# Performance work log

Measured on AMD Instinct MI355X. Metric: run time of the kernel, lower is better.

## Reference

```python
import jax, jax.numpy as jnp
import numpy as np

N, E, C, D_E, G = 50000, 800000, 64, 32, 512


def setup_inputs() -> dict:
    key = jax.random.key(0)
    ks = jax.random.split(key, 12)
    inp = {
        "x": jax.random.normal(ks[0], (N, C), dtype=jnp.float32),
        "edge_index": jax.random.randint(ks[1], (2, E), 0, N, dtype=jnp.int64),
        "edge_attr": jax.random.normal(ks[2], (E, D_E), dtype=jnp.float32),
        "batch": jnp.sort(jax.random.randint(ks[3], (N,), 0, G, dtype=jnp.int64)),
        "num_graphs": G,
        # CGConv gating linears: Linear(2*C + D_E, C)
        "W_f": jax.random.normal(ks[4], (2 * C + D_E, C), dtype=jnp.float32) * 0.05,
        "b_f": jnp.zeros((C,), dtype=jnp.float32),
        "W_s": jax.random.normal(ks[5], (2 * C + D_E, C), dtype=jnp.float32) * 0.05,
        "b_s": jnp.zeros((C,), dtype=jnp.float32),
        # head MLP
        "W1": jax.random.normal(ks[6], (C, 6), dtype=jnp.float32) * 0.1,
        "b1": jnp.zeros((6,), dtype=jnp.float32),
        "W2": jax.random.normal(ks[7], (6, 1), dtype=jnp.float32) * 0.1,
        "b2": jnp.zeros((1,), dtype=jnp.float32),
    }
    return inp


def cg_conv(x, edge_index, edge_attr, W_f, b_f, W_s, b_s):
    src, dst = edge_index[0], edge_index[1]
    # PyG CGConv message: z = cat([x_i (dst), x_j (src), edge_attr])
    z = jnp.concatenate([x[dst], x[src], edge_attr], axis=-1)  # [E, 2C+D]
    msg = jax.nn.sigmoid(z @ W_f + b_f) * jax.nn.softplus(z @ W_s + b_s)  # [E, C]
    agg = jax.ops.segment_sum(msg, dst, num_segments=x.shape[0])  # scatter-add to dst
    return x + agg  # residual


def reference(x, edge_index, edge_attr, batch, num_graphs, W_f, b_f, W_s, b_s, W1, b1, W2, b2):
    h = cg_conv(x, edge_index, edge_attr, W_f, b_f, W_s, b_s)  # [N, C]
    h = jax.nn.sigmoid(h)
    h = jax.nn.sigmoid(h @ W1 + b1)  # [N, 6]
    g = jax.ops.segment_sum(h, batch, num_segments=num_graphs)  # global_add_pool [G, 6]
    out = jax.nn.relu(g @ W2 + b2)  # [G, 1]
    return out
```

## Files before the change

### kernel.cpp

```cpp
#include <hip/hip_runtime.h>
#include <hip/hip_bf16.h>
#include <stdint.h>

#define NN 50000
#define EE 800000
#define CC 64
#define DE 32
#define KD 160
#define NC 128
#define GG 512
#define SCAN_B 1024
#define NSCAN ((NN + SCAN_B - 1) / SCAN_B)

typedef __attribute__((ext_vector_type(8))) short bf16x8;
typedef __attribute__((ext_vector_type(4))) float f32x4;

__device__ __forceinline__ float sigmoidf_(float v) {
  return __fdividef(1.f, 1.f + __expf(-v));
}
__device__ __forceinline__ float softplusf_(float v) {
  return fmaxf(v, 0.f) + __logf(1.f + __expf(-fabsf(v)));
}
__device__ __forceinline__ unsigned short f2bf(float f) {
  uint32_t u = __float_as_uint(f);
  return (unsigned short)((u + 0x7FFFu + ((u >> 16) & 1u)) >> 16);
}
__device__ __forceinline__ float bf2f(unsigned short h) {
  return __uint_as_float(((uint32_t)h) << 16);
}
__device__ __forceinline__ void tsplit(float f, short& hi, short& lo) {
  uint32_t u = __float_as_uint(f);
  float lf = f - __uint_as_float(u & 0xFFFF0000u);
  hi = (short)(u >> 16);
  lo = (short)(__float_as_uint(lf) >> 16);
}

__global__ void count_kernel(const int* __restrict__ ei, int* __restrict__ deg) {
  int e = blockIdx.x * 256 + threadIdx.x;
  atomicAdd(&deg[ei[EE + e]], 1);
}

__global__ __launch_bounds__(SCAN_B) void scan1_kernel(
    const int* __restrict__ deg, int* __restrict__ pos, int* __restrict__ bsum) {
  __shared__ int s[SCAN_B];
  int t = threadIdx.x, i = blockIdx.x * SCAN_B + t;
  s[t] = (i < NN) ? deg[i] : 0;
  __syncthreads();
  for (int off = 1; off < SCAN_B; off <<= 1) {
    int a = (t >= off) ? s[t - off] : 0;
    __syncthreads();
    s[t] += a;
    __syncthreads();
  }
  if (i < NN) pos[i + 1] = s[t];
  if (t == SCAN_B - 1) bsum[blockIdx.x] = s[t];
}

__global__ void scan2_kernel(int* __restrict__ bsum) {
  __shared__ int s[64];
  int t = threadIdx.x;
  s[t] = (t < NSCAN) ? bsum[t] : 0;
  __syncthreads();
  for (int off = 1; off < 64; off <<= 1) {
    int a = (t >= off) ? s[t - off] : 0;
    __syncthreads();
    s[t] += a;
    __syncthreads();
  }
  bsum[t] = (t == 0) ? 0 : s[t - 1];
}

__global__ __launch_bounds__(SCAN_B) void scan3_kernel(
    int* __restrict__ pos, const int* __restrict__ bsum, int* __restrict__ cursor) {
  int t = threadIdx.x, i = blockIdx.x * SCAN_B + t;
  if (i < NN) {
    int v = pos[i + 1] + bsum[blockIdx.x];
    pos[i + 1] = v;
    if (i + 1 < NN) cursor[i + 1] = v;
  }
  if (i == 0) { pos[0] = 0; cursor[0] = 0; }
}

__global__ void fill_kernel(const int* __restrict__ ei, int* __restrict__ cursor,
                            int* __restrict__ eidx, int* __restrict__ dsts,
                            int* __restrict__ srcs) {
  int e = blockIdx.x * 256 + threadIdx.x;
  int d = ei[EE + e];
  int s = ei[e];
  int slot = atomicAdd(&cursor[d], 1);
  eidx[slot] = e;
  dsts[slot] = d;
  srcs[slot] = s;
}

__global__ void xsplit_kernel(const float* __restrict__ x,
                              unsigned short* __restrict__ xhi,
                              unsigned short* __restrict__ xlo) {
  int idx = blockIdx.x * 256 + threadIdx.x;
  float4 v = ((const float4*)x)[idx];
  ushort4 h, l;
  short a, b;
  tsplit(v.x, a, b); h.x = (unsigned short)a; l.x = (unsigned short)b;
  tsplit(v.y, a, b); h.y = (unsigned short)a; l.y = (unsigned short)b;
  tsplit(v.z, a, b); h.z = (unsigned short)a; l.z = (unsigned short)b;
  tsplit(v.w, a, b); h.w = (unsigned short)a; l.w = (unsigned short)b;
  *(ushort4*)(xhi + (size_t)idx * 4) = h;
  *(ushort4*)(xlo + (size_t)idx * 4) = l;
}

__global__ void wprep_kernel(const float* __restrict__ Wf, const float* __restrict__ Ws,
                             short* __restrict__ Bph, short* __restrict__ Bpl) {
  int p = blockIdx.x * 256 + threadIdx.x;
  int i = p & 7, l = (p >> 3) & 63, tile = p >> 9;
  int nt = tile & 7, s = tile >> 3;
  int k = s * 32 + 8 * (l >> 4) + i;
  int col = nt * 16 + (l & 15);
  float w = (col < CC) ? Wf[k * CC + col] : Ws[k * CC + (col - CC)];
  short hi, lo;
  tsplit(w, hi, lo);
  Bph[p] = hi;
  Bpl[p] = lo;
}

template <bool BF16MSG>
__global__ __launch_bounds__(512) void edge_mfma_kernel(
    const unsigned short* __restrict__ xhi, const unsigned short* __restrict__ xlo,
    const int* __restrict__ eidx, const int* __restrict__ dsts,
    const int* __restrict__ srcs, const float* __restrict__ ea,
    const short* __restrict__ Bph, const short* __restrict__ Bpl,
    const float* __restrict__ bfv, const float* __restrict__ bsv,
    void* __restrict__ msg)
{
  __shared__ short Bh[20480];
  const int t = threadIdx.x;

  {
    const float4* gh = (const float4*)Bph;
    float4* sh = (float4*)Bh;
    #pragma unroll
    for (int r = 0; r < 5; ++r) sh[r * 512 + t] = gh[r * 512 + t];
  }

  const int w  = t >> 6, l = t & 63;
  const int mg = w >> 1, ng = w & 1;
  const int sbase = blockIdx.x * 256 + mg * 64;
  const int lr = l & 15, lg = l >> 4;

  int dst[4], src[4], ep[4];
  #pragma unroll
  for (int mt = 0; mt < 4; ++mt) {
    const int slot = sbase + mt * 16 + lr;
    dst[mt] = dsts[slot];
    src[mt] = srcs[slot];
    ep[mt]  = eidx[slot];
  }
  __syncthreads();

  f32x4 acc[4][4];
  #pragma unroll
  for (int mt = 0; mt < 4; ++mt)
    #pragma unroll
    for (int q = 0; q < 4; ++q) acc[mt][q] = (f32x4){0.f, 0.f, 0.f, 0.f};

  const bf16x8* Blg = (const bf16x8*)Bpl;

  #pragma unroll
  for (int s = 0; s < 5; ++s) {
    bf16x8 ah[4], al[4];
    if (s < 4) {
      const int koff = (s & 1) * 32 + 8 * lg;
      #pragma unroll
      for (int mt = 0; mt < 4; ++mt) {
        const int row = (s < 2) ? dst[mt] : src[mt];
        const size_t o = (size_t)row * CC + koff;
        ah[mt] = *(const bf16x8*)(xhi + o);
        al[mt] = *(const bf16x8*)(xlo + o);
      }
    } else {
      #pragma unroll
      for (int mt = 0; mt < 4; ++mt) {
        const float4* p4 = (const float4*)(ea + (size_t)ep[mt] * DE + 8 * lg);
        float4 v0 = p4[0], v1 = p4[1];
        float v[8] = {v0.x, v0.y, v0.z, v0.w, v1.x, v1.y, v1.z, v1.w};
        #pragma unroll
        for (int i = 0; i < 8; ++i) {
          short hh, ll;
          tsplit(v[i], hh, ll);
          ah[mt][i] = hh;
          al[mt][i] = ll;
        }
      }
    }
    bf16x8 bh[4], bl[4];
    #pragma unroll
    for (int q = 0; q < 4; ++q) {
      const int nt  = 2 * ng + (q & 1) + (q >> 1) * 4;
      bh[q] = *(const bf16x8*)(Bh + ((s * 8 + nt) * 64 + l) * 8);
      bl[q] = Blg[(s * 8 + nt) * 64 + l];
    }
    #pragma unroll
    for (int mt = 0; mt < 4; ++mt)
      #pragma unroll
      for (int q = 0; q < 4; ++q)
        acc[mt][q] = __builtin_amdgcn_mfma_f32_16x16x32_bf16(ah[mt], bh[q], acc[mt][q], 0, 0, 0);
    #pragma unroll
    for (int mt = 0; mt < 4; ++mt)
      #pragma unroll
      for (int q = 0; q < 4; ++q)
        acc[mt][q] = __builtin_amdgcn_mfma_f32_16x16x32_bf16(al[mt], bh[q], acc[mt][q], 0, 0, 0);
    #pragma unroll
    for (int mt = 0; mt < 4; ++mt)
      #pragma unroll
      for (int q = 0; q < 4; ++q)
        acc[mt][q] = __builtin_amdgcn_mfma_f32_16x16x32_bf16(ah[mt], bl[q], acc[mt][q], 0, 0, 0);
  }

  #pragma unroll
  for (int p2 = 0; p2 < 2; ++p2) {
    const int ch = (2 * ng + p2) * 16 + lr;
    const float bF = bfv[ch], bS = bsv[ch];
    #pragma unroll
    for (int mt = 0; mt < 4; ++mt) {
      f32x4 F = acc[mt][p2];
      f32x4 S = acc[mt][p2 + 2];
      #pragma unroll
      for (int r = 0; r < 4; ++r) {
        const int oslot = sbase + mt * 16 + lg * 4 + r;
        const float mval = sigmoidf_(F[r] + bF) * softplusf_(S[r] + bS);
        if constexpr (!BF16MSG) {
          ((float*)msg)[(size_t)oslot * CC + ch] = mval;
        } else {
          ((unsigned short*)msg)[(size_t)oslot * CC + ch] = f2bf(mval);
        }
      }
    }
  }
}

template <bool BF16MSG>
__global__ __launch_bounds__(256) void gather_node_kernel(
    const void* __restrict__ msg, const int* __restrict__ pos,
    const float* __restrict__ x, const int* __restrict__ batch,
    const float* __restrict__ W1, const float* __restrict__ b1,
    float* __restrict__ pool)
{
  const int t = threadIdx.x;
  const int n = blockIdx.x * 16 + (t >> 4);
  const int i = t & 15;
  const int start = pos[n], end = pos[n + 1];

  float4 acc = make_float4(0.f, 0.f, 0.f, 0.f);
  if constexpr (!BF16MSG) {
    const float4* m4 = (const float4*)msg;
    for (int p = start; p < end; ++p) {
      float4 m = m4[(size_t)p * 16 + i];
      acc.x += m.x; acc.y += m.y; acc.z += m.z; acc.w += m.w;
    }
  } else {
    const unsigned short* mb = (const unsigned short*)msg;
    for (int p = start; p < end; ++p) {
      ushort4 u = *(const ushort4*)(mb + (size_t)p * CC + 4 * i);
      acc.x += bf2f(u.x); acc.y += bf2f(u.y); acc.z += bf2f(u.z); acc.w += bf2f(u.w);
    }
  }

  const float4 xv = *(const float4*)(x + (size_t)n * CC + 4 * i);
  float h0 = sigmoidf_(xv.x + acc.x);
  float h1 = sigmoidf_(xv.y + acc.y);
  float h2 = sigmoidf_(xv.z + acc.z);
  float h3 = sigmoidf_(xv.w + acc.w);

  float o[6];
  const float* wp = W1 + (size_t)(4 * i) * 6;
  #pragma unroll
  for (int j = 0; j < 6; ++j) {
    o[j] = h0 * wp[j] + h1 * wp[6 + j] + h2 * wp[12 + j] + h3 * wp[18 + j];
  }
  #pragma unroll
  for (int d = 8; d > 0; d >>= 1) {
    #pragma unroll
    for (int j = 0; j < 6; ++j) o[j] += __shfl_down(o[j], d, 16);
  }
  if (i == 0) {
    int g = batch[n];
    #pragma unroll
    for (int j = 0; j < 6; ++j)
      atomicAdd(&pool[g * 6 + j], sigmoidf_(o[j] + b1[j]));
  }
}

__global__ void out_kernel(const float* __restrict__ pool,
                           const float* __restrict__ W2,
                           const float* __restrict__ b2,
                           float* __restrict__ out)
{
  int g = blockIdx.x * 64 + threadIdx.x;
  if (g < GG) {
    float acc = b2[0];
    #pragma unroll
    for (int j = 0; j < 6; ++j) acc = fmaf(pool[g * 6 + j], W2[j], acc);
    out[g] = fmaxf(acc, 0.f);
  }
}

static inline size_t al64(size_t v) { return (v + 63) & ~(size_t)63; }

extern "C" void kernel_launch(void* const* d_in, const int* in_sizes, int n_in,
                              void* d_out, int out_size, void* d_ws, size_t ws_size,
                              hipStream_t stream) {
  const float* x     = (const float*)d_in[0];
  const int*   ei    = (const int*)d_in[1];
  const float* ea    = (const float*)d_in[2];
  const int*   batch = (const int*)d_in[3];
  const float* Wf = (const float*)d_in[5];
  const float* bf = (const float*)d_in[6];
  const float* Ws = (const float*)d_in[7];
  const float* bs = (const float*)d_in[8];
  const float* W1 = (const float*)d_in[9];
  const float* b1 = (const float*)d_in[10];
  const float* W2 = (const float*)d_in[11];
  const float* b2 = (const float*)d_in[12];
  float* out = (float*)d_out;

  const size_t fixed = al64((size_t)NN * CC * 2) * 2 +
                       al64((size_t)KD * NC * 2) * 2 +
                       al64((size_t)NN * 4) + al64((size_t)(NN + 1) * 4) +
                       al64((size_t)NN * 4) + al64(64 * 4) +
                       al64((size_t)EE * 4) * 3 +
                       al64((size_t)GG * 6 * 4);
  const bool f32 = ws_size >= al64((size_t)EE * CC * 4) + fixed;

  char* p = (char*)d_ws;
  void* msg = (void*)p;
  p += al64(f32 ? (size_t)EE * CC * 4 : (size_t)EE * CC * 2);
  unsigned short* xhi = (unsigned short*)p; p += al64((size_t)NN * CC * 2);
  unsigned short* xlo = (unsigned short*)p; p += al64((size_t)NN * CC * 2);
  short* Bph = (short*)p; p += al64((size_t)KD * NC * 2);
  short* Bpl = (short*)p; p += al64((size_t)KD * NC * 2);
  int* deg    = (int*)p; p += al64((size_t)NN * 4);
  int* pos    = (int*)p; p += al64((size_t)(NN + 1) * 4);
  int* cursor = (int*)p; p += al64((size_t)NN * 4);
  int* bsum   = (int*)p; p += al64(64 * 4);
  int* eidx   = (int*)p; p += al64((size_t)EE * 4);
  int* dsts   = (int*)p; p += al64((size_t)EE * 4);
  int* srcs   = (int*)p; p += al64((size_t)EE * 4);
  float* pool = (float*)p;

  hipMemsetAsync(deg, 0, (size_t)NN * 4, stream);
  hipMemsetAsync(pool, 0, (size_t)GG * 6 * 4, stream);

  xsplit_kernel<<<NN * CC / 4 / 256, 256, 0, stream>>>(x, xhi, xlo);
  wprep_kernel<<<KD * NC / 256, 256, 0, stream>>>(Wf, Ws, Bph, Bpl);

  count_kernel<<<EE / 256, 256, 0, stream>>>(ei, deg);
  scan1_kernel<<<NSCAN, SCAN_B, 0, stream>>>(deg, pos, bsum);
  scan2_kernel<<<1, 64, 0, stream>>>(bsum);
  scan3_kernel<<<NSCAN, SCAN_B, 0, stream>>>(pos, bsum, cursor);
  fill_kernel<<<EE / 256, 256, 0, stream>>>(ei, cursor, eidx, dsts, srcs);

  if (f32) {
    edge_mfma_kernel<false><<<EE / 256, 512, 0, stream>>>(xhi, xlo, eidx, dsts, srcs, ea, Bph, Bpl, bf, bs, msg);
    gather_node_kernel<false><<<NN / 16, 256, 0, stream>>>(msg, pos, x, batch, W1, b1, pool);
  } else {
    edge_mfma_kernel<true><<<EE / 256, 512, 0, stream>>>(xhi, xlo, eidx, dsts, srcs, ea, Bph, Bpl, bf, bs, msg);
    gather_node_kernel<true><<<NN / 16, 256, 0, stream>>>(msg, pos, x, batch, W1, b1, pool);
  }
  out_kernel<<<(GG + 63) / 64, 64, 0, stream>>>(pool, W2, b2, out);
}
```

Measured before the change: 561.2 us.

## Fuse scan and prep kernels, pre-split edge attrs, retile node gather

Replaces the three-pass scan with a single-block wave-shuffle scan and merges the x-split and weight-prep kernels into one launch. Adds a pass that gathers edge_attr into CSR order already split into bf16 hi/lo, so the edge MFMA kernel reads it contiguously instead of converting it inline. Reworks the node gather to 8 lanes per node with a one-step prefetch. Drops the bf16 message fallback and always assumes a fp32 message buffer. The costs are an extra full pass over edge_attr and a serial single-block scan.

```diff
diff --git a/kernel.cpp b/kernel.cpp
--- a/kernel.cpp
+++ b/kernel.cpp
@@ -9,8 +9,6 @@
 #define KD 160
 #define NC 128
 #define GG 512
-#define SCAN_B 1024
-#define NSCAN ((NN + SCAN_B - 1) / SCAN_B)
 
 typedef __attribute__((ext_vector_type(8))) short bf16x8;
 typedef __attribute__((ext_vector_type(4))) float f32x4;
@@ -20,13 +18,6 @@
 }
 __device__ __forceinline__ float softplusf_(float v) {
   return fmaxf(v, 0.f) + __logf(1.f + __expf(-fabsf(v)));
-}
-__device__ __forceinline__ unsigned short f2bf(float f) {
-  uint32_t u = __float_as_uint(f);
-  return (unsigned short)((u + 0x7FFFu + ((u >> 16) & 1u)) >> 16);
-}
-__device__ __forceinline__ float bf2f(unsigned short h) {
-  return __uint_as_float(((uint32_t)h) << 16);
 }
 __device__ __forceinline__ void tsplit(float f, short& hi, short& lo) {
   uint32_t u = __float_as_uint(f);
@@ -40,45 +31,42 @@
   atomicAdd(&deg[ei[EE + e]], 1);
 }
 
-__global__ __launch_bounds__(SCAN_B) void scan1_kernel(
-    const int* __restrict__ deg, int* __restrict__ pos, int* __restrict__ bsum) {
-  __shared__ int s[SCAN_B];
-  int t = threadIdx.x, i = blockIdx.x * SCAN_B + t;
-  s[t] = (i < NN) ? deg[i] : 0;
-  __syncthreads();
-  for (int off = 1; off < SCAN_B; off <<= 1) {
-    int a = (t >= off) ? s[t - off] : 0;
+__global__ __launch_bounds__(1024) void scan_fused_kernel(
+    const int* __restrict__ deg, int* __restrict__ pos, int* __restrict__ cursor) {
+  __shared__ int ws[16];
+  const int t = threadIdx.x;
+  const int lane = t & 63, wv = t >> 6;
+  int carry = 0;
+  if (t == 0) { pos[0] = 0; cursor[0] = 0; }
+  for (int base = 0; base < NN; base += 1024) {
+    const int i = base + t;
+    int v = (i < NN) ? deg[i] : 0;
+    #pragma unroll
+    for (int off = 1; off < 64; off <<= 1) {
+      int u = __shfl_up(v, off, 64);
+      if (lane >= off) v += u;
+    }
+    if (lane == 63) ws[wv] = v;
     __syncthreads();
-    s[t] += a;
+    if (wv == 0 && lane < 16) {
+      int s = ws[lane];
+      #pragma unroll
+      for (int off = 1; off < 16; off <<= 1) {
+        int u = __shfl_up(s, off, 64);
+        if (lane >= off) s += u;
+      }
+      ws[lane] = s;
+    }
     __syncthreads();
-  }
-  if (i < NN) pos[i + 1] = s[t];
-  if (t == SCAN_B - 1) bsum[blockIdx.x] = s[t];
-}
-
-__global__ void scan2_kernel(int* __restrict__ bsum) {
-  __shared__ int s[64];
-  int t = threadIdx.x;
-  s[t] = (t < NSCAN) ? bsum[t] : 0;
-  __syncthreads();
-  for (int off = 1; off < 64; off <<= 1) {
-    int a = (t >= off) ? s[t - off] : 0;
+    const int add = (wv > 0 ? ws[wv - 1] : 0) + carry;
+    if (i < NN) {
+      const int incl = v + add;
+      pos[i + 1] = incl;
+      if (i < NN - 1) cursor[i + 1] = incl;
+    }
+    carry += ws[15];
     __syncthreads();
-    s[t] += a;
-    __syncthreads();
-  }
-  bsum[t] = (t == 0) ? 0 : s[t - 1];
-}
-
-__global__ __launch_bounds__(SCAN_B) void scan3_kernel(
-    int* __restrict__ pos, const int* __restrict__ bsum, int* __restrict__ cursor) {
-  int t = threadIdx.x, i = blockIdx.x * SCAN_B + t;
-  if (i < NN) {
-    int v = pos[i + 1] + bsum[blockIdx.x];
-    pos[i + 1] = v;
-    if (i + 1 < NN) cursor[i + 1] = v;
-  }
-  if (i == 0) { pos[0] = 0; cursor[0] = 0; }
+  }
 }
 
 __global__ void fill_kernel(const int* __restrict__ ei, int* __restrict__ cursor,
@@ -93,43 +81,69 @@
   srcs[slot] = s;
 }
 
-__global__ void xsplit_kernel(const float* __restrict__ x,
-                              unsigned short* __restrict__ xhi,
-                              unsigned short* __restrict__ xlo) {
-  int idx = blockIdx.x * 256 + threadIdx.x;
-  float4 v = ((const float4*)x)[idx];
-  ushort4 h, l;
-  short a, b;
-  tsplit(v.x, a, b); h.x = (unsigned short)a; l.x = (unsigned short)b;
-  tsplit(v.y, a, b); h.y = (unsigned short)a; l.y = (unsigned short)b;
-  tsplit(v.z, a, b); h.z = (unsigned short)a; l.z = (unsigned short)b;
-  tsplit(v.w, a, b); h.w = (unsigned short)a; l.w = (unsigned short)b;
-  *(ushort4*)(xhi + (size_t)idx * 4) = h;
-  *(ushort4*)(xlo + (size_t)idx * 4) = l;
-}
-
-__global__ void wprep_kernel(const float* __restrict__ Wf, const float* __restrict__ Ws,
-                             short* __restrict__ Bph, short* __restrict__ Bpl) {
-  int p = blockIdx.x * 256 + threadIdx.x;
-  int i = p & 7, l = (p >> 3) & 63, tile = p >> 9;
-  int nt = tile & 7, s = tile >> 3;
-  int k = s * 32 + 8 * (l >> 4) + i;
-  int col = nt * 16 + (l & 15);
-  float w = (col < CC) ? Wf[k * CC + col] : Ws[k * CC + (col - CC)];
-  short hi, lo;
-  tsplit(w, hi, lo);
-  Bph[p] = hi;
-  Bpl[p] = lo;
-}
-
-template <bool BF16MSG>
+__global__ void xsplit_wprep_kernel(const float* __restrict__ x,
+                                    unsigned short* __restrict__ xhi,
+                                    unsigned short* __restrict__ xlo,
+                                    const float* __restrict__ Wf,
+                                    const float* __restrict__ Ws,
+                                    short* __restrict__ Bph,
+                                    short* __restrict__ Bpl) {
+  if (blockIdx.x < 3125) {
+    int idx = blockIdx.x * 256 + threadIdx.x;
+    float4 v = ((const float4*)x)[idx];
+    ushort4 h, l;
+    short a, b;
+    tsplit(v.x, a, b); h.x = (unsigned short)a; l.x = (unsigned short)b;
+    tsplit(v.y, a, b); h.y = (unsigned short)a; l.y = (unsigned short)b;
+    tsplit(v.z, a, b); h.z = (unsigned short)a; l.z = (unsigned short)b;
+    tsplit(v.w, a, b); h.w = (unsigned short)a; l.w = (unsigned short)b;
+    *(ushort4*)(xhi + (size_t)idx * 4) = h;
+    *(ushort4*)(xlo + (size_t)idx * 4) = l;
+  } else {
+    int p = (blockIdx.x - 3125) * 256 + threadIdx.x;
+    int i = p & 7, l = (p >> 3) & 63, tile = p >> 9;
+    int nt = tile & 7, s = tile >> 3;
+    int k = s * 32 + 8 * (l >> 4) + i;
+    int col = nt * 16 + (l & 15);
+    float w = (col < CC) ? Wf[k * CC + col] : Ws[k * CC + (col - CC)];
+    short hi, lo;
+    tsplit(w, hi, lo);
+    Bph[p] = hi;
+    Bpl[p] = lo;
+  }
+}
+
+__global__ void eaprep_kernel(const float* __restrict__ ea,
+                              const int* __restrict__ eidx,
+                              unsigned short* __restrict__ eap) {
+  int tid = blockIdx.x * 256 + threadIdx.x;
+  int slot = tid >> 2, c = tid & 3;
+  int e = eidx[slot];
+  const float4* s4 = (const float4*)(ea + (size_t)e * DE + c * 8);
+  float4 a = s4[0], b = s4[1];
+  float v[8] = {a.x, a.y, a.z, a.w, b.x, b.y, b.z, b.w};
+  bf16x8 h, l;
+  #pragma unroll
+  for (int i = 0; i < 8; ++i) {
+    short hh, ll;
+    tsplit(v[i], hh, ll);
+    h[i] = hh;
+    l[i] = ll;
+  }
+  unsigned short* o = eap + (size_t)slot * 64 + c * 16;
+  *(bf16x8*)o = h;
+  *(bf16x8*)(o + 8) = l;
+}
+
+template <bool EAP>
 __global__ __launch_bounds__(512) void edge_mfma_kernel(
     const unsigned short* __restrict__ xhi, const unsigned short* __restrict__ xlo,
+    const unsigned short* __restrict__ eap,
     const int* __restrict__ eidx, const int* __restrict__ dsts,
     const int* __restrict__ srcs, const float* __restrict__ ea,
     const short* __restrict__ Bph, const short* __restrict__ Bpl,
     const float* __restrict__ bfv, const float* __restrict__ bsv,
-    void* __restrict__ msg)
+    float* __restrict__ msg)
 {
   __shared__ short Bh[20480];
   const int t = threadIdx.x;
@@ -152,7 +166,7 @@
     const int slot = sbase + mt * 16 + lr;
     dst[mt] = dsts[slot];
     src[mt] = srcs[slot];
-    ep[mt]  = eidx[slot];
+    if constexpr (!EAP) ep[mt] = eidx[slot];
   }
   __syncthreads();
 
@@ -175,6 +189,13 @@
         const size_t o = (size_t)row * CC + koff;
         ah[mt] = *(const bf16x8*)(xhi + o);
         al[mt] = *(const bf16x8*)(xlo + o);
+      }
+    } else if constexpr (EAP) {
+      #pragma unroll
+      for (int mt = 0; mt < 4; ++mt) {
+        const unsigned short* o = eap + (size_t)(sbase + mt * 16 + lr) * 64 + lg * 16;
+        ah[mt] = *(const bf16x8*)o;
+        al[mt] = *(const bf16x8*)(o + 8);
       }
     } else {
       #pragma unroll
@@ -194,7 +215,7 @@
     bf16x8 bh[4], bl[4];
     #pragma unroll
     for (int q = 0; q < 4; ++q) {
-      const int nt  = 2 * ng + (q & 1) + (q >> 1) * 4;
+      const int nt = 2 * ng + (q & 1) + (q >> 1) * 4;
       bh[q] = *(const bf16x8*)(Bh + ((s * 8 + nt) * 64 + l) * 8);
       bl[q] = Blg[(s * 8 + nt) * 64 + l];
     }
@@ -226,60 +247,63 @@
       #pragma unroll
       for (int r = 0; r < 4; ++r) {
         const int oslot = sbase + mt * 16 + lg * 4 + r;
-        const float mval = sigmoidf_(F[r] + bF) * softplusf_(S[r] + bS);
-        if constexpr (!BF16MSG) {
-          ((float*)msg)[(size_t)oslot * CC + ch] = mval;
-        } else {
-          ((unsigned short*)msg)[(size_t)oslot * CC + ch] = f2bf(mval);
-        }
-      }
-    }
-  }
-}
-
-template <bool BF16MSG>
+        msg[(size_t)oslot * CC + ch] = sigmoidf_(F[r] + bF) * softplusf_(S[r] + bS);
+      }
+    }
+  }
+}
+
 __global__ __launch_bounds__(256) void gather_node_kernel(
-    const void* __restrict__ msg, const int* __restrict__ pos,
+    const float* __restrict__ msg, const int* __restrict__ pos,
     const float* __restrict__ x, const int* __restrict__ batch,
     const float* __restrict__ W1, const float* __restrict__ b1,
     float* __restrict__ pool)
 {
   const int t = threadIdx.x;
-  const int n = blockIdx.x * 16 + (t >> 4);
-  const int i = t & 15;
+  const int n = blockIdx.x * 32 + (t >> 3);
+  if (n >= NN) return;
+  const int i = t & 7;
   const int start = pos[n], end = pos[n + 1];
 
-  float4 acc = make_float4(0.f, 0.f, 0.f, 0.f);
-  if constexpr (!BF16MSG) {
-    const float4* m4 = (const float4*)msg;
-    for (int p = start; p < end; ++p) {
-      float4 m = m4[(size_t)p * 16 + i];
-      acc.x += m.x; acc.y += m.y; acc.z += m.z; acc.w += m.w;
-    }
-  } else {
-    const unsigned short* mb = (const unsigned short*)msg;
-    for (int p = start; p < end; ++p) {
-      ushort4 u = *(const ushort4*)(mb + (size_t)p * CC + 4 * i);
-      acc.x += bf2f(u.x); acc.y += bf2f(u.y); acc.z += bf2f(u.z); acc.w += bf2f(u.w);
-    }
-  }
-
-  const float4 xv = *(const float4*)(x + (size_t)n * CC + 4 * i);
-  float h0 = sigmoidf_(xv.x + acc.x);
-  float h1 = sigmoidf_(xv.y + acc.y);
-  float h2 = sigmoidf_(xv.z + acc.z);
-  float h3 = sigmoidf_(xv.w + acc.w);
+  float4 a0 = make_float4(0.f, 0.f, 0.f, 0.f);
+  float4 a1 = make_float4(0.f, 0.f, 0.f, 0.f);
+  const float4* m4 = (const float4*)msg;
+  float4 c0, c1;
+  if (start < end) {
+    c0 = m4[(size_t)start * 16 + 2 * i];
+    c1 = m4[(size_t)start * 16 + 2 * i + 1];
+  }
+  for (int p = start; p < end; ++p) {
+    float4 u0 = c0, u1 = c1;
+    if (p + 1 < end) {
+      c0 = m4[(size_t)(p + 1) * 16 + 2 * i];
+      c1 = m4[(size_t)(p + 1) * 16 + 2 * i + 1];
+    }
+    a0.x += u0.x; a0.y += u0.y; a0.z += u0.z; a0.w += u0.w;
+    a1.x += u1.x; a1.y += u1.y; a1.z += u1.z; a1.w += u1.w;
+  }
+
+  const float4 x0 = *(const float4*)(x + (size_t)n * CC + 8 * i);
+  const float4 x1 = *(const float4*)(x + (size_t)n * CC + 8 * i + 4);
+  float h[8];
+  h[0] = sigmoidf_(x0.x + a0.x); h[1] = sigmoidf_(x0.y + a0.y);
+  h[2] = sigmoidf_(x0.z + a0.z); h[3] = sigmoidf_(x0.w + a0.w);
+  h[4] = sigmoidf_(x1.x + a1.x); h[5] = sigmoidf_(x1.y + a1.y);
+  h[6] = sigmoidf_(x1.z + a1.z); h[7] = sigmoidf_(x1.w + a1.w);
 
   float o[6];
-  const float* wp = W1 + (size_t)(4 * i) * 6;
-  #pragma unroll
-  for (int j = 0; j < 6; ++j) {
-    o[j] = h0 * wp[j] + h1 * wp[6 + j] + h2 * wp[12 + j] + h3 * wp[18 + j];
-  }
-  #pragma unroll
-  for (int d = 8; d > 0; d >>= 1) {
-    #pragma unroll
-    for (int j = 0; j < 6; ++j) o[j] += __shfl_down(o[j], d, 16);
+  #pragma unroll
+  for (int j = 0; j < 6; ++j) o[j] = 0.f;
+  #pragma unroll
+  for (int c = 0; c < 8; ++c) {
+    const float* wp = W1 + (size_t)(8 * i + c) * 6;
+    #pragma unroll
+    for (int j = 0; j < 6; ++j) o[j] = fmaf(h[c], wp[j], o[j]);
+  }
+  #pragma unroll
+  for (int d = 4; d > 0; d >>= 1) {
+    #pragma unroll
+    for (int j = 0; j < 6; ++j) o[j] += __shfl_down(o[j], d, 8);
   }
   if (i == 0) {
     int g = batch[n];
@@ -322,48 +346,39 @@
   const float* b2 = (const float*)d_in[12];
   float* out = (float*)d_out;
 
-  const size_t fixed = al64((size_t)NN * CC * 2) * 2 +
-                       al64((size_t)KD * NC * 2) * 2 +
-                       al64((size_t)NN * 4) + al64((size_t)(NN + 1) * 4) +
-                       al64((size_t)NN * 4) + al64(64 * 4) +
-                       al64((size_t)EE * 4) * 3 +
-                       al64((size_t)GG * 6 * 4);
-  const bool f32 = ws_size >= al64((size_t)EE * CC * 4) + fixed;
-
   char* p = (char*)d_ws;
-  void* msg = (void*)p;
-  p += al64(f32 ? (size_t)EE * CC * 4 : (size_t)EE * CC * 2);
+  float* msg = (float*)p;            p += al64((size_t)EE * CC * 4);
   unsigned short* xhi = (unsigned short*)p; p += al64((size_t)NN * CC * 2);
   unsigned short* xlo = (unsigned short*)p; p += al64((size_t)NN * CC * 2);
-  short* Bph = (short*)p; p += al64((size_t)KD * NC * 2);
-  short* Bpl = (short*)p; p += al64((size_t)KD * NC * 2);
-  int* deg    = (int*)p; p += al64((size_t)NN * 4);
-  int* pos    = (int*)p; p += al64((size_t)(NN + 1) * 4);
-  int* cursor = (int*)p; p += al64((size_t)NN * 4);
-  int* bsum   = (int*)p; p += al64(64 * 4);
-  int* eidx   = (int*)p; p += al64((size_t)EE * 4);
-  int* dsts   = (int*)p; p += al64((size_t)EE * 4);
-  int* srcs   = (int*)p; p += al64((size_t)EE * 4);
-  float* pool = (float*)p;
+  short* Bph = (short*)p;            p += al64((size_t)KD * NC * 2);
+  short* Bpl = (short*)p;            p += al64((size_t)KD * NC * 2);
+  int* deg    = (int*)p;             p += al64((size_t)NN * 4);
+  int* pos    = (int*)p;             p += al64((size_t)(NN + 1) * 4);
+  int* cursor = (int*)p;             p += al64((size_t)NN * 4);
+  int* eidx   = (int*)p;             p += al64((size_t)EE * 4);
+  int* dsts   = (int*)p;             p += al64((size_t)EE * 4);
+  int* srcs   = (int*)p;             p += al64((size_t)EE * 4);
+  float* pool = (float*)p;           p += al64((size_t)GG * 6 * 4);
+  unsigned short* eap = (unsigned short*)p;
+  const bool use_eap =
+      ((size_t)(p - (char*)d_ws) + al64((size_t)EE * 64 * 2)) <= ws_size;
 
   hipMemsetAsync(deg, 0, (size_t)NN * 4, stream);
   hipMemsetAsync(pool, 0, (size_t)GG * 6 * 4, stream);
 
-  xsplit_kernel<<<NN * CC / 4 / 256, 256, 0, stream>>>(x, xhi, xlo);
-  wprep_kernel<<<KD * NC / 256, 256, 0, stream>>>(Wf, Ws, Bph, Bpl);
-
+  xsplit_wprep_kernel<<<3205, 256, 0, stream>>>(x, xhi, xlo, Wf, Ws, Bph, Bpl);
   count_kernel<<<EE / 256, 256, 0, stream>>>(ei, deg);
-  scan1_kernel<<<NSCAN, SCAN_B, 0, stream>>>(deg, pos, bsum);
-  scan2_kernel<<<1, 64, 0, stream>>>(bsum);
-  scan3_kernel<<<NSCAN, SCAN_B, 0, stream>>>(pos, bsum, cursor);
+  scan_fused_kernel<<<1, 1024, 0, stream>>>(deg, pos, cursor);
   fill_kernel<<<EE / 256, 256, 0, stream>>>(ei, cursor, eidx, dsts, srcs);
 
-  if (f32) {
-    edge_mfma_kernel<false><<<EE / 256, 512, 0, stream>>>(xhi, xlo, eidx, dsts, srcs, ea, Bph, Bpl, bf, bs, msg);
-    gather_node_kernel<false><<<NN / 16, 256, 0, stream>>>(msg, pos, x, batch, W1, b1, pool);
+  if (use_eap) {
+    eaprep_kernel<<<EE * 4 / 256, 256, 0, stream>>>(ea, eidx, eap);
+    edge_mfma_kernel<true><<<EE / 256, 512, 0, stream>>>(
+        xhi, xlo, eap, eidx, dsts, srcs, ea, Bph, Bpl, bf, bs, msg);
   } else {
-    edge_mfma_kernel<true><<<EE / 256, 512, 0, stream>>>(xhi, xlo, eidx, dsts, srcs, ea, Bph, Bpl, bf, bs, msg);
-    gather_node_kernel<true><<<NN / 16, 256, 0, stream>>>(msg, pos, x, batch, W1, b1, pool);
-  }
+    edge_mfma_kernel<false><<<EE / 256, 512, 0, stream>>>(
+        xhi, xlo, eap, eidx, dsts, srcs, ea, Bph, Bpl, bf, bs, msg);
+  }
+  gather_node_kernel<<<(NN + 31) / 32, 256, 0, stream>>>(msg, pos, x, batch, W1, b1, pool);
   out_kernel<<<(GG + 63) / 64, 64, 0, stream>>>(pool, W2, b2, out);
 }
```

Result: slower. 610.6 us (+8.8%).
